# Kernel tuning notes

Hardware: AMD Instinct MI355X
Metric: run time of the kernel (lower is better)

## Reference

```python
import jax, jax.numpy as jnp
import numpy as np

# Dimensions derived from Mamba.__init__: d_model=512 -> joint_latent=32, mamb_latent=D=640
NL, D, DIN, DS, DTR, DC = 4, 640, 1280, 16, 40, 4  # n_layer, d_model, d_inner, d_state, dt_rank, d_conv
B, V = 64, 30  # batch, joint-sequence length (repeat_joint_num)


def _rms(x, w, eps=1e-5):
    return x * jax.lax.rsqrt(jnp.mean(x * x, axis=-1, keepdims=True) + eps) * w


def _mamba_block(x, in_w, conv_w, conv_b, xp_w, dt_w, dt_b, A_log, D_skip, out_w):
    # x: [B, V, D]
    u, res = jnp.split(jnp.einsum('bvd,ed->bve', x, in_w), 2, axis=-1)  # each [B,V,DIN]
    # causal depthwise conv1d over V
    xc = jnp.pad(u.transpose(0, 2, 1), ((0, 0), (0, 0), (DC - 1, 0)))  # [B,DIN,V+DC-1]
    xc = jax.lax.conv_general_dilated(xc, conv_w[:, None, :], (1,), 'VALID',
                                      feature_group_count=DIN,
                                      dimension_numbers=('NCH', 'OIH', 'NCH'))
    u = jax.nn.silu(xc.transpose(0, 2, 1) + conv_b)  # [B,V,DIN]
    # input-dependent SSM params
    dbl = jnp.einsum('bvd,ed->bve', u, xp_w)  # [B,V,DTR+2*DS]
    delta, Bm, Cm = jnp.split(dbl, [DTR, DTR + DS], axis=-1)
    delta = jax.nn.softplus(jnp.einsum('bvr,dr->bvd', delta, dt_w) + dt_b)  # [B,V,DIN]
    A = -jnp.exp(A_log)  # [DIN,DS]
    dA = jnp.exp(delta[..., None] * A)                              # [B,V,DIN,DS]
    dBu = delta[..., None] * Bm[:, :, None, :] * u[..., None]       # [B,V,DIN,DS]

    def step(h, t):
        dA_t, dBu_t, C_t = t
        h = dA_t * h + dBu_t                      # [B,DIN,DS]
        return h, jnp.einsum('bds,bs->bd', h, C_t)

    h0 = jnp.zeros((x.shape[0], DIN, DS), x.dtype)
    _, ys = jax.lax.scan(step, h0, (dA.transpose(1, 0, 2, 3),
                                    dBu.transpose(1, 0, 2, 3),
                                    Cm.transpose(1, 0, 2)))
    y = ys.transpose(1, 0, 2) + u * D_skip        # [B,V,DIN]
    return jnp.einsum('bvd,ed->bve', y * jax.nn.silu(res), out_w)


def setup_inputs() -> dict:
    key = jax.random.key(0)
    ks = jax.random.split(key, 10)
    s = 0.02
    return {
        'x': jax.random.normal(ks[0], (B, V, D), jnp.float32),
        'vs': jax.random.randint(ks[1], (B,), 0, V),
        'norm_w': jnp.ones((NL, D), jnp.float32),
        'in_proj_w': s * jax.random.normal(ks[2], (NL, 2 * DIN, D), jnp.float32),
        'conv_w': s * jax.random.normal(ks[3], (NL, DIN, DC), jnp.float32),
        'conv_b': jnp.zeros((NL, DIN), jnp.float32),
        'x_proj_w': s * jax.random.normal(ks[4], (NL, DTR + 2 * DS, DIN), jnp.float32),
        'dt_proj_w': s * jax.random.normal(ks[5], (NL, DIN, DTR), jnp.float32),
        'dt_proj_b': jnp.full((NL, DIN), -4.0, jnp.float32) + 0.1 * jax.random.normal(ks[6], (NL, DIN), jnp.float32),
        'A_log': jnp.tile(jnp.log(jnp.arange(1.0, DS + 1.0, dtype=jnp.float32)), (NL, DIN, 1)),
        'D_skip': jnp.ones((NL, DIN), jnp.float32),
        'out_proj_w': s * jax.random.normal(ks[7], (NL, D, DIN), jnp.float32),
        'norm_f_w': jnp.ones((D,), jnp.float32),
    }


def reference(x, vs, norm_w, in_proj_w, conv_w, conv_b, x_proj_w, dt_proj_w,
              dt_proj_b, A_log, D_skip, out_proj_w, norm_f_w):
    bidx = jnp.arange(x.shape[0])[:, None]
    # batch-wise circular permutation over V (circular_permute_v)
    fwd_idx = (jnp.arange(V)[None, :] + V - vs[:, None]) % V  # [B,V]
    h = x[bidx, fwd_idx]
    for i in range(NL):
        h = h + _mamba_block(_rms(h, norm_w[i]), in_proj_w[i], conv_w[i], conv_b[i],
                             x_proj_w[i], dt_proj_w[i], dt_proj_b[i], A_log[i],
                             D_skip[i], out_proj_w[i])
    h = _rms(h, norm_f_w)
    # reverse_circular_permute_v
    rev_idx = (jnp.arange(V)[None, :] + vs[:, None]) % V
    return h[bidx, rev_idx]
```

## Files before the change

kernel.cpp:

```cpp
#include <hip/hip_runtime.h>
#include <math.h>

#define NLAYER 4
#define DMODEL 640
#define DINNER 1280
#define DSTATE 16
#define DTRANK 40
#define DCONV  4
#define BATCH  64
#define SEQ    30
#define MTOK   (BATCH*SEQ)
#define NPROJ  (2*DINNER)
#define NDBL   (DTRANK+2*DSTATE)
#define NDBLP  80
#define KSEGS  8
#define KSEG   (DINNER/KSEGS)
#define DTKP   64

#define Q1 (NLAYER*NPROJ*DMODEL/4)
#define Q2 (NLAYER*DMODEL*DINNER/4)
#define Q3 (NLAYER*NDBLP*DINNER/4)
#define Q4 (NLAYER*DINNER*DTKP/4)
#define WCTOT (Q1+Q2+Q3+Q4)

typedef unsigned short u16;
typedef __bf16 bf16x8 __attribute__((ext_vector_type(8)));
typedef float  f32x4  __attribute__((ext_vector_type(4)));
typedef unsigned short u16x8 __attribute__((ext_vector_type(8)));

__device__ __forceinline__ float siluf(float x) {
    return x / (1.0f + __expf(-x));
}

__device__ __forceinline__ u16 f2bf(float f) {
    unsigned int u = __float_as_uint(f);
    u += 0x7fffu + ((u >> 16) & 1u);
    return (u16)(u >> 16);
}

__device__ __forceinline__ float bf2f(u16 b) {
    return __uint_as_float(((unsigned int)b) << 16);
}

__global__ void k_permute(const float* __restrict__ x, const int* __restrict__ vs,
                          float* __restrict__ h) {
    int idx = blockIdx.x * blockDim.x + threadIdx.x;
    if (idx >= MTOK * DMODEL) return;
    int d  = idx % DMODEL;
    int mv = idx / DMODEL;
    int v  = mv % SEQ;
    int b  = mv / SEQ;
    int src = (v + SEQ - vs[b]) % SEQ;
    h[idx] = x[(b * SEQ + src) * DMODEL + d];
}

__global__ __launch_bounds__(256)
void k_wconv(const float* __restrict__ in_w, const float* __restrict__ out_w,
             const float* __restrict__ xp_w, const float* __restrict__ dt_w,
             u16* __restrict__ wbi, u16* __restrict__ wbo,
             u16* __restrict__ wbx, u16* __restrict__ wdt) {
    int i = blockIdx.x * 256 + threadIdx.x;
    if (i < Q1) {
        int j = i * 4;
        float4 v = *(const float4*)(in_w + j);
        ushort4 o;
        o.x = f2bf(v.x); o.y = f2bf(v.y); o.z = f2bf(v.z); o.w = f2bf(v.w);
        *(ushort4*)(wbi + j) = o;
    } else if (i < Q1 + Q2) {
        int j = (i - Q1) * 4;
        float4 v = *(const float4*)(out_w + j);
        ushort4 o;
        o.x = f2bf(v.x); o.y = f2bf(v.y); o.z = f2bf(v.z); o.w = f2bf(v.w);
        *(ushort4*)(wbo + j) = o;
    } else if (i < Q1 + Q2 + Q3) {
        int j = (i - Q1 - Q2) * 4;
        int layer = j / (NDBLP * DINNER);
        int rem   = j % (NDBLP * DINNER);
        int r = rem / DINNER, c = rem % DINNER;
        ushort4 o = make_ushort4(0, 0, 0, 0);
        if (r < NDBL) {
            float4 v = *(const float4*)(xp_w + ((size_t)layer * NDBL + r) * DINNER + c);
            o.x = f2bf(v.x); o.y = f2bf(v.y); o.z = f2bf(v.z); o.w = f2bf(v.w);
        }
        *(ushort4*)(wbx + j) = o;
    } else {
        int j = (i - Q1 - Q2 - Q3) * 4;
        int ld = j / DTKP;
        int c  = j % DTKP;
        ushort4 o = make_ushort4(0, 0, 0, 0);
        if (c < DTRANK) {
            float4 v = *(const float4*)(dt_w + (size_t)ld * DTRANK + c);
            o.x = f2bf(v.x); o.y = f2bf(v.y); o.z = f2bf(v.z); o.w = f2bf(v.w);
        }
        *(ushort4*)(wdt + j) = o;
    }
}

__global__ __launch_bounds__(64)
void k_rmsnorm(const float* __restrict__ h, const float* __restrict__ w,
               u16* __restrict__ xn) {
    int m = blockIdx.x;
    int t = threadIdx.x;
    const float* row = h + (size_t)m * DMODEL;
    float2 vv[5];
    float ss = 0.f;
    #pragma unroll
    for (int i = 0; i < 5; ++i) {
        vv[i] = *(const float2*)(row + i * 128 + t * 2);
        ss += vv[i].x * vv[i].x + vv[i].y * vv[i].y;
    }
    #pragma unroll
    for (int o = 32; o > 0; o >>= 1) ss += __shfl_xor(ss, o, 64);
    float sc = rsqrtf(ss / DMODEL + 1e-5f);
    u16* outp = xn + (size_t)m * DMODEL;
    #pragma unroll
    for (int i = 0; i < 5; ++i) {
        int d = i * 128 + t * 2;
        float2 wv = *(const float2*)(w + d);
        ushort2 o;
        o.x = f2bf(vv[i].x * sc * wv.x);
        o.y = f2bf(vv[i].y * sc * wv.y);
        *(ushort2*)(outp + d) = o;
    }
}

__global__ __launch_bounds__(256)
void k_inproj(const u16* __restrict__ A, const u16* __restrict__ W,
              u16* __restrict__ Cb) {
    __shared__ u16 As[2][64 * 64];
    __shared__ u16 Bs[2][128 * 64];
    const int t = threadIdx.x;
    const int w = t >> 6, l = t & 63;
    const int lane15 = l & 15, quad = l >> 4;
    const int wm = w >> 1, wn = w & 1;
    const int m0 = blockIdx.y * 64, n0 = blockIdx.x * 128;

    f32x4 acc[2][4];
    #pragma unroll
    for (int i = 0; i < 2; ++i)
        #pragma unroll
        for (int j = 0; j < 4; ++j)
            acc[i][j] = (f32x4){0.f, 0.f, 0.f, 0.f};

    auto stage = [&](int buf, int k0) {
        #pragma unroll
        for (int q = 0; q < 2; ++q) {
            int c   = q * 256 + t;
            int row = c >> 3;
            int gch = ((c & 7) ^ (row & 7)) * 8;
            const u16* ga = A + (size_t)(m0 + row) * DMODEL + k0 + gch;
            __builtin_amdgcn_global_load_lds(
                (const __attribute__((address_space(1))) void*)ga,
                (__attribute__((address_space(3))) void*)&As[buf][c * 8], 16, 0, 0);
        }
        #pragma unroll
        for (int q = 0; q < 4; ++q) {
            int c   = q * 256 + t;
            int row = c >> 3;
            int gch = ((c & 7) ^ (row & 7)) * 8;
            const u16* gb = W + (size_t)(n0 + row) * DMODEL + k0 + gch;
            __builtin_amdgcn_global_load_lds(
                (const __attribute__((address_space(1))) void*)gb,
                (__attribute__((address_space(3))) void*)&Bs[buf][c * 8], 16, 0, 0);
        }
    };

    auto compute = [&](int buf) {
        #pragma unroll
        for (int ks = 0; ks < 2; ++ks) {
            bf16x8 af[2], bfr[4];
            #pragma unroll
            for (int i = 0; i < 2; ++i) {
                int row = wm * 32 + i * 16 + lane15;
                af[i] = *(const bf16x8*)&As[buf][row * 64 + (((ks * 4 + quad) ^ (row & 7)) * 8)];
            }
            #pragma unroll
            for (int j = 0; j < 4; ++j) {
                int row = wn * 64 + j * 16 + lane15;
                bfr[j] = *(const bf16x8*)&Bs[buf][row * 64 + (((ks * 4 + quad) ^ (row & 7)) * 8)];
            }
            #pragma unroll
            for (int i = 0; i < 2; ++i)
                #pragma unroll
                for (int j = 0; j < 4; ++j)
                    acc[i][j] = __builtin_amdgcn_mfma_f32_16x16x32_bf16(
                        af[i], bfr[j], acc[i][j], 0, 0, 0);
        }
    };

    const int NT = DMODEL / 64;
    stage(0, 0);
    __syncthreads();
    int cur = 0;
    for (int tt = 1; tt < NT; ++tt) {
        stage(cur ^ 1, tt * 64);
        compute(cur);
        __syncthreads();
        cur ^= 1;
    }
    compute(cur);

    #pragma unroll
    for (int i = 0; i < 2; ++i) {
        #pragma unroll
        for (int r = 0; r < 4; ++r) {
            int row = m0 + wm * 32 + i * 16 + quad * 4 + r;
            #pragma unroll
            for (int j = 0; j < 4; ++j) {
                int col = n0 + wn * 64 + j * 16 + lane15;
                Cb[(size_t)row * NPROJ + col] = f2bf(acc[i][j][r]);
            }
        }
    }
}

__global__ __launch_bounds__(128)
void k_outproj(const u16* __restrict__ A, const u16* __restrict__ W,
               const float* __restrict__ resid, float* __restrict__ C) {
    __shared__ u16 As[2][32 * 128];
    __shared__ u16 Bs[2][64 * 128];
    const int t = threadIdx.x;
    const int w = t >> 6, l = t & 63;
    const int lane15 = l & 15, quad = l >> 4;
    const int m0 = blockIdx.y * 32, n0 = blockIdx.x * 64;

    f32x4 acc[2][2];
    #pragma unroll
    for (int i = 0; i < 2; ++i)
        #pragma unroll
        for (int j = 0; j < 2; ++j)
            acc[i][j] = (f32x4){0.f, 0.f, 0.f, 0.f};

    auto stage = [&](int buf, int k0) {
        #pragma unroll
        for (int q = 0; q < 4; ++q) {
            int c   = q * 128 + t;
            int row = c >> 4;
            int gch = ((c & 15) ^ (row & 15)) * 8;
            const u16* ga = A + (size_t)(m0 + row) * DINNER + k0 + gch;
            __builtin_amdgcn_global_load_lds(
                (const __attribute__((address_space(1))) void*)ga,
                (__attribute__((address_space(3))) void*)&As[buf][c * 8], 16, 0, 0);
        }
        #pragma unroll
        for (int q = 0; q < 8; ++q) {
            int c   = q * 128 + t;
            int row = c >> 4;
            int gch = ((c & 15) ^ (row & 15)) * 8;
            const u16* gb = W + (size_t)(n0 + row) * DINNER + k0 + gch;
            __builtin_amdgcn_global_load_lds(
                (const __attribute__((address_space(1))) void*)gb,
                (__attribute__((address_space(3))) void*)&Bs[buf][c * 8], 16, 0, 0);
        }
    };

    auto compute = [&](int buf) {
        #pragma unroll
        for (int ks = 0; ks < 4; ++ks) {
            bf16x8 af[2], bfr[2];
            #pragma unroll
            for (int i = 0; i < 2; ++i) {
                int row = i * 16 + lane15;
                af[i] = *(const bf16x8*)&As[buf][row * 128 + (((ks * 4 + quad) ^ (row & 15)) * 8)];
            }
            #pragma unroll
            for (int j = 0; j < 2; ++j) {
                int row = w * 32 + j * 16 + lane15;
                bfr[j] = *(const bf16x8*)&Bs[buf][row * 128 + (((ks * 4 + quad) ^ (row & 15)) * 8)];
            }
            #pragma unroll
            for (int i = 0; i < 2; ++i)
                #pragma unroll
                for (int j = 0; j < 2; ++j)
                    acc[i][j] = __builtin_amdgcn_mfma_f32_16x16x32_bf16(
                        af[i], bfr[j], acc[i][j], 0, 0, 0);
        }
    };

    const int NT = DINNER / 128;
    stage(0, 0);
    __syncthreads();
    int cur = 0;
    for (int tt = 1; tt < NT; ++tt) {
        stage(cur ^ 1, tt * 128);
        compute(cur);
        __syncthreads();
        cur ^= 1;
    }
    compute(cur);

    #pragma unroll
    for (int i = 0; i < 2; ++i) {
        #pragma unroll
        for (int r = 0; r < 4; ++r) {
            int row = m0 + i * 16 + quad * 4 + r;
            #pragma unroll
            for (int j = 0; j < 2; ++j) {
                int col = n0 + w * 32 + j * 16 + lane15;
                size_t idx = (size_t)row * DMODEL + col;
                C[idx] = acc[i][j][r] + resid[idx];
            }
        }
    }
}

__global__ __launch_bounds__(256)
void k_conv(const u16* __restrict__ urb, const float* __restrict__ cw,
            const float* __restrict__ cb, u16* __restrict__ ubf) {
    int idx = blockIdx.x * 256 + threadIdx.x;
    int c = idx % DINNER;
    int b = idx / DINNER;
    const u16* up = urb + (size_t)(b * SEQ) * NPROJ + c;
    float xv[SEQ];
    #pragma unroll
    for (int v = 0; v < SEQ; ++v) xv[v] = bf2f(up[(size_t)v * NPROJ]);
    float w0 = cw[c * 4 + 0], w1 = cw[c * 4 + 1];
    float w2 = cw[c * 4 + 2], w3 = cw[c * 4 + 3];
    float bias = cb[c];
    u16* op = ubf + (size_t)(b * SEQ) * DINNER + c;
    float x0 = 0.f, x1 = 0.f, x2 = 0.f;
    #pragma unroll
    for (int v = 0; v < SEQ; ++v) {
        float x3 = xv[v];
        float o = bias + w0 * x0 + w1 * x1 + w2 * x2 + w3 * x3;
        op[(size_t)v * DINNER] = f2bf(siluf(o));
        x0 = x1; x1 = x2; x2 = x3;
    }
}

__global__ __launch_bounds__(256)
void k_xproj(const u16* __restrict__ ubf, const u16* __restrict__ wbx,
             float* __restrict__ dblp) {
    __shared__ u16 As[64 * KSEG];
    __shared__ u16 Bs[NDBLP * KSEG];
    const int t = threadIdx.x;
    const int w = t >> 6, l = t & 63;
    const int lane15 = l & 15, quad = l >> 4;
    const int seg = blockIdx.x;
    const int m0 = blockIdx.y * 64;
    const int kb = seg * KSEG;

    #pragma unroll
    for (int q = 0; q < 5; ++q) {
        int c   = q * 256 + t;
        int row = c / 20, ch = c - row * 20;
        const u16* ga = ubf + (size_t)(m0 + row) * DINNER + kb + ch * 8;
        __builtin_amdgcn_global_load_lds(
            (const __attribute__((address_space(1))) void*)ga,
            (__attribute__((address_space(3))) void*)&As[c * 8], 16, 0, 0);
    }
    #pragma unroll
    for (int q = 0; q < 6; ++q) {
        int c   = q * 256 + t;
        int row = c / 20, ch = c - row * 20;
        const u16* gb = wbx + (size_t)row * DINNER + kb + ch * 8;
        __builtin_amdgcn_global_load_lds(
            (const __attribute__((address_space(1))) void*)gb,
            (__attribute__((address_space(3))) void*)&Bs[c * 8], 16, 0, 0);
    }
    if (t < 64) {
        int c   = 1536 + t;
        int row = c / 20, ch = c - row * 20;
        const u16* gb = wbx + (size_t)row * DINNER + kb + ch * 8;
        __builtin_amdgcn_global_load_lds(
            (const __attribute__((address_space(1))) void*)gb,
            (__attribute__((address_space(3))) void*)&Bs[c * 8], 16, 0, 0);
    }
    __syncthreads();

    f32x4 acc[5];
    #pragma unroll
    for (int j = 0; j < 5; ++j) acc[j] = (f32x4){0.f, 0.f, 0.f, 0.f};

    #pragma unroll
    for (int k0 = 0; k0 < KSEG; k0 += 32) {
        bf16x8 af = *(const bf16x8*)&As[(w * 16 + lane15) * KSEG + k0 + quad * 8];
        #pragma unroll
        for (int j = 0; j < 5; ++j) {
            bf16x8 bfrag = *(const bf16x8*)&Bs[(j * 16 + lane15) * KSEG + k0 + quad * 8];
            acc[j] = __builtin_amdgcn_mfma_f32_16x16x32_bf16(af, bfrag, acc[j], 0, 0, 0);
        }
    }

    float* outp = dblp + (size_t)seg * MTOK * NDBLP;
    #pragma unroll
    for (int r = 0; r < 4; ++r) {
        int row = m0 + w * 16 + quad * 4 + r;
        #pragma unroll
        for (int j = 0; j < 5; ++j) {
            int col = j * 16 + lane15;
            outp[(size_t)row * NDBLP + col] = acc[j][r];
        }
    }
}

__global__ __launch_bounds__(256)
void k_dtgemm(const float* __restrict__ dblp, const u16* __restrict__ dtwb,
              const float* __restrict__ dtb, u16* __restrict__ delta) {
    __shared__ u16 As[2][64 * 32];
    __shared__ u16 Bs[2][64 * 32];
    const int t = threadIdx.x;
    const int w = t >> 6, l = t & 63;
    const int lane15 = l & 15, quad = l >> 4;
    const int wm = w >> 1, wn = w & 1;
    const int m0 = blockIdx.y * 64, n0 = blockIdx.x * 64;
    const int row = t >> 2, koff = (t & 3) * 8;
    const int m = m0 + row;

    #pragma unroll
    for (int kt = 0; kt < 2; ++kt) {
        int c = t;
        const u16* gb = dtwb + (size_t)(n0 + (c >> 2)) * DTKP + kt * 32 + (c & 3) * 8;
        __builtin_amdgcn_global_load_lds(
            (const __attribute__((address_space(1))) void*)gb,
            (__attribute__((address_space(3))) void*)&Bs[kt][c * 8], 16, 0, 0);
    }

    float sums[2][8];
    #pragma unroll
    for (int kt = 0; kt < 2; ++kt)
        #pragma unroll
        for (int e = 0; e < 8; ++e) sums[kt][e] = 0.f;
    #pragma unroll
    for (int kt = 0; kt < 2; ++kt) {
        #pragma unroll
        for (int q = 0; q < 2; ++q) {
            int col = kt * 32 + koff + q * 4;
            if (col < DTRANK) {
                #pragma unroll
                for (int sg = 0; sg < KSEGS; ++sg) {
                    float4 p = *(const float4*)&dblp[(size_t)sg * MTOK * NDBLP
                                                     + (size_t)m * NDBLP + col];
                    sums[kt][q * 4 + 0] += p.x; sums[kt][q * 4 + 1] += p.y;
                    sums[kt][q * 4 + 2] += p.z; sums[kt][q * 4 + 3] += p.w;
                }
            }
        }
    }
    #pragma unroll
    for (int kt = 0; kt < 2; ++kt) {
        u16x8 av;
        #pragma unroll
        for (int e = 0; e < 8; ++e) av[e] = f2bf(sums[kt][e]);
        *(u16x8*)&As[kt][row * 32 + koff] = av;
    }
    __syncthreads();

    f32x4 acc[2][2];
    #pragma unroll
    for (int i = 0; i < 2; ++i)
        #pragma unroll
        for (int j = 0; j < 2; ++j)
            acc[i][j] = (f32x4){0.f, 0.f, 0.f, 0.f};

    #pragma unroll
    for (int kt = 0; kt < 2; ++kt) {
        bf16x8 af[2], bfrag[2];
        #pragma unroll
        for (int i = 0; i < 2; ++i)
            af[i] = *(const bf16x8*)&As[kt][(wm * 32 + i * 16 + lane15) * 32 + quad * 8];
        #pragma unroll
        for (int j = 0; j < 2; ++j)
            bfrag[j] = *(const bf16x8*)&Bs[kt][(wn * 32 + j * 16 + lane15) * 32 + quad * 8];
        #pragma unroll
        for (int i = 0; i < 2; ++i)
            #pragma unroll
            for (int j = 0; j < 2; ++j)
                acc[i][j] = __builtin_amdgcn_mfma_f32_16x16x32_bf16(
                    af[i], bfrag[j], acc[i][j], 0, 0, 0);
    }

    #pragma unroll
    for (int i = 0; i < 2; ++i) {
        #pragma unroll
        for (int r = 0; r < 4; ++r) {
            int orow = m0 + wm * 32 + i * 16 + quad * 4 + r;
            #pragma unroll
            for (int j = 0; j < 2; ++j) {
                int col = n0 + wn * 32 + j * 16 + lane15;
                float vv = acc[i][j][r] + dtb[col];
                vv = (vv > 20.f) ? vv : log1pf(__expf(vv));
                delta[(size_t)orow * DINNER + col] = f2bf(vv);
            }
        }
    }
}

__global__ __launch_bounds__(256)
void k_scan(const u16* __restrict__ ubf, const u16* __restrict__ urb,
            const float* __restrict__ dblp, const u16* __restrict__ delta,
            const float* __restrict__ A_log, const float* __restrict__ Dsk,
            u16* __restrict__ y) {
    __shared__ float BC[SEQ][2 * DSTATE];
    const int b  = blockIdx.x / (DINNER / 128);
    const int dc = blockIdx.x % (DINNER / 128);
    const int dloc = threadIdx.x >> 1;
    const int half = threadIdx.x & 1;
    const int d  = dc * 128 + dloc;

    for (int t = threadIdx.x; t < SEQ * 2 * DSTATE; t += 256) {
        int v = t >> 5, s = t & 31;
        float acc = 0.f;
        #pragma unroll
        for (int sg = 0; sg < KSEGS; ++sg)
            acc += dblp[(size_t)sg * MTOK * NDBLP + (size_t)(b * SEQ + v) * NDBLP + DTRANK + s];
        BC[v][s] = acc;
    }
    __syncthreads();

    float dl[SEQ], uu[SEQ], rr[SEQ];
    #pragma unroll
    for (int v = 0; v < SEQ; ++v)
        dl[v] = bf2f(delta[(size_t)(b * SEQ + v) * DINNER + d]);
    #pragma unroll
    for (int v = 0; v < SEQ; ++v)
        uu[v] = bf2f(ubf[(size_t)(b * SEQ + v) * DINNER + d]);
    #pragma unroll
    for (int v = 0; v < SEQ; ++v)
        rr[v] = bf2f(urb[(size_t)(b * SEQ + v) * NPROJ + DINNER + d]);

    float Ar[8];
    #pragma unroll
    for (int s = 0; s < 8; ++s)
        Ar[s] = -__expf(A_log[(size_t)d * DSTATE + half * 8 + s]);
    float dsk = Dsk[d];
    float st8[8];
    #pragma unroll
    for (int s = 0; s < 8; ++s) st8[s] = 0.f;

    u16* yp = y + (size_t)(b * SEQ) * DINNER + d;

    #pragma unroll
    for (int v = 0; v < SEQ; ++v) {
        float dlt = dl[v];
        float du  = dlt * uu[v];
        float ya = 0.f, yb = 0.f;
        #pragma unroll
        for (int s = 0; s < 8; s += 4) {
            float dA0 = __expf(dlt * Ar[s + 0]);
            float dA1 = __expf(dlt * Ar[s + 1]);
            float dA2 = __expf(dlt * Ar[s + 2]);
            float dA3 = __expf(dlt * Ar[s + 3]);
            st8[s + 0] = dA0 * st8[s + 0] + du * BC[v][half * 8 + s + 0];
            st8[s + 1] = dA1 * st8[s + 1] + du * BC[v][half * 8 + s + 1];
            st8[s + 2] = dA2 * st8[s + 2] + du * BC[v][half * 8 + s + 2];
            st8[s + 3] = dA3 * st8[s + 3] + du * BC[v][half * 8 + s + 3];
            ya += st8[s + 0] * BC[v][DSTATE + half * 8 + s + 0];
            yb += st8[s + 1] * BC[v][DSTATE + half * 8 + s + 1];
            ya += st8[s + 2] * BC[v][DSTATE + half * 8 + s + 2];
            yb += st8[s + 3] * BC[v][DSTATE + half * 8 + s + 3];
        }
        float yh = ya + yb;
        yh += __shfl_xor(yh, 1, 64);
        if (half == 0)
            yp[(size_t)v * DINNER] = f2bf((yh + uu[v] * dsk) * siluf(rr[v]));
    }
}

__global__ __launch_bounds__(64)
void k_final(const float* __restrict__ h, const int* __restrict__ vs,
             const float* __restrict__ w, float* __restrict__ out) {
    int mv = blockIdx.x;
    int v = mv % SEQ, b = mv / SEQ;
    int src = (v + vs[b]) % SEQ;
    const float* row = h + (size_t)(b * SEQ + src) * DMODEL;
    int t = threadIdx.x;
    float ss = 0.f;
    for (int d = t; d < DMODEL; d += 64) { float x = row[d]; ss += x * x; }
    #pragma unroll
    for (int o = 32; o > 0; o >>= 1) ss += __shfl_xor(ss, o, 64);
    float sc = rsqrtf(ss / DMODEL + 1e-5f);
    float* op = out + (size_t)mv * DMODEL;
    for (int d = t; d < DMODEL; d += 64) op[d] = row[d] * sc * w[d];
}

extern "C" void kernel_launch(void* const* d_in, const int* in_sizes, int n_in,
                              void* d_out, int out_size, void* d_ws, size_t ws_size,
                              hipStream_t stream) {
    const float* x      = (const float*)d_in[0];
    const int*   vs     = (const int*)d_in[1];
    const float* norm_w = (const float*)d_in[2];
    const float* in_w   = (const float*)d_in[3];
    const float* conv_w = (const float*)d_in[4];
    const float* conv_b = (const float*)d_in[5];
    const float* xp_w   = (const float*)d_in[6];
    const float* dt_w   = (const float*)d_in[7];
    const float* dt_b   = (const float*)d_in[8];
    const float* A_log  = (const float*)d_in[9];
    const float* Dsk    = (const float*)d_in[10];
    const float* out_w  = (const float*)d_in[11];
    const float* nfw    = (const float*)d_in[12];
    float* out = (float*)d_out;

    char* p = (char*)d_ws;
    float* h      = (float*)p; p += (size_t)MTOK * DMODEL * 4;
    u16*   xn     = (u16*)p;   p += (size_t)MTOK * DMODEL * 2;
    u16*   urb    = (u16*)p;   p += (size_t)MTOK * NPROJ * 2;
    u16*   ubf    = (u16*)p;   p += (size_t)MTOK * DINNER * 2;
    float* dblp   = (float*)p; p += (size_t)KSEGS * MTOK * NDBLP * 4;
    u16*   deltab = (u16*)p;   p += (size_t)MTOK * DINNER * 2;
    u16*   y      = (u16*)p;   p += (size_t)MTOK * DINNER * 2;
    u16*   wbi4   = (u16*)p;   p += (size_t)NLAYER * NPROJ * DMODEL * 2;
    u16*   wbo4   = (u16*)p;   p += (size_t)NLAYER * DMODEL * DINNER * 2;
    u16*   wbx4   = (u16*)p;   p += (size_t)NLAYER * NDBLP * DINNER * 2;
    u16*   wdt4   = (u16*)p;   p += (size_t)NLAYER * DINNER * DTKP * 2;

    k_wconv<<<WCTOT / 256, 256, 0, stream>>>(
        in_w, out_w, xp_w, dt_w, wbi4, wbo4, wbx4, wdt4);

    k_permute<<<(MTOK * DMODEL + 255) / 256, 256, 0, stream>>>(x, vs, h);

    for (int l = 0; l < NLAYER; ++l) {
        k_rmsnorm<<<MTOK, 64, 0, stream>>>(h, norm_w + (size_t)l * DMODEL, xn);

        k_inproj<<<dim3(NPROJ / 128, MTOK / 64), 256, 0, stream>>>(
            xn, wbi4 + (size_t)l * NPROJ * DMODEL, urb);

        k_conv<<<BATCH * DINNER / 256, 256, 0, stream>>>(
            urb, conv_w + (size_t)l * DINNER * DCONV, conv_b + (size_t)l * DINNER, ubf);

        k_xproj<<<dim3(KSEGS, MTOK / 64), 256, 0, stream>>>(
            ubf, wbx4 + (size_t)l * NDBLP * DINNER, dblp);

        k_dtgemm<<<dim3(DINNER / 64, MTOK / 64), 256, 0, stream>>>(
            dblp, wdt4 + (size_t)l * DINNER * DTKP,
            dt_b + (size_t)l * DINNER, deltab);

        k_scan<<<BATCH * (DINNER / 128), 256, 0, stream>>>(
            ubf, urb, dblp, deltab,
            A_log + (size_t)l * DINNER * DSTATE, Dsk + (size_t)l * DINNER, y);

        k_outproj<<<dim3(DMODEL / 64, MTOK / 32), 128, 0, stream>>>(
            y, wbo4 + (size_t)l * DMODEL * DINNER, h, h);
    }

    k_final<<<MTOK, 64, 0, stream>>>(h, vs, nfw, out);
}
```

Before: 441.4 us.

## Fuse dt-projection GEMM with selective scan into one kernel

Merges the dt_proj GEMM (with softplus) and the selective-scan kernel into a single kernel, so each block computes delta for 60 tokens (two batches) by 64 channels and keeps it in shared memory. The scan then reads delta, u and the gate res from LDS instead of global memory, and the bf16 delta buffer is removed. This saves one launch plus the write and re-read of delta. In exchange each block uses more LDS, the GEMM runs on 60 valid rows padded to 64 (clamped row index), and the grid shape changes.

```diff
diff --git a/kernel.cpp b/kernel.cpp
--- a/kernel.cpp
+++ b/kernel.cpp
@@ -395,17 +395,25 @@
 }
 
 __global__ __launch_bounds__(256)
-void k_dtgemm(const float* __restrict__ dblp, const u16* __restrict__ dtwb,
-              const float* __restrict__ dtb, u16* __restrict__ delta) {
+void k_dtscan(const float* __restrict__ dblp, const u16* __restrict__ dtwb,
+              const float* __restrict__ dtb,
+              const u16* __restrict__ ubf, const u16* __restrict__ urb,
+              const float* __restrict__ A_log, const float* __restrict__ Dsk,
+              u16* __restrict__ y) {
     __shared__ u16 As[2][64 * 32];
     __shared__ u16 Bs[2][64 * 32];
+    __shared__ u16 ldelta[64][64];
+    __shared__ float BC2[2][SEQ][32];
+    __shared__ u16 UU[60 * 64];
+    __shared__ u16 RR[60 * 64];
     const int t = threadIdx.x;
     const int w = t >> 6, l = t & 63;
     const int lane15 = l & 15, quad = l >> 4;
     const int wm = w >> 1, wn = w & 1;
-    const int m0 = blockIdx.y * 64, n0 = blockIdx.x * 64;
+    const int n0 = blockIdx.x * 64;
+    const int m0 = blockIdx.y * 60;
     const int row = t >> 2, koff = (t & 3) * 8;
-    const int m = m0 + row;
+    const int mm = min(m0 + row, MTOK - 1);
 
     #pragma unroll
     for (int kt = 0; kt < 2; ++kt) {
@@ -415,6 +423,28 @@
             (const __attribute__((address_space(1))) void*)gb,
             (__attribute__((address_space(3))) void*)&Bs[kt][c * 8], 16, 0, 0);
     }
+    for (int o = t; o < 480; o += 256) {
+        int rr_ = o >> 3, ch = o & 7;
+        const u16* g1 = ubf + (size_t)(m0 + rr_) * DINNER + n0 + ch * 8;
+        __builtin_amdgcn_global_load_lds(
+            (const __attribute__((address_space(1))) void*)g1,
+            (__attribute__((address_space(3))) void*)&UU[o * 8], 16, 0, 0);
+        const u16* g2 = urb + (size_t)(m0 + rr_) * NPROJ + DINNER + n0 + ch * 8;
+        __builtin_amdgcn_global_load_lds(
+            (const __attribute__((address_space(1))) void*)g2,
+            (__attribute__((address_space(3))) void*)&RR[o * 8], 16, 0, 0);
+    }
+    for (int s0 = t; s0 < 2 * SEQ * 32; s0 += 256) {
+        int lb  = s0 / (SEQ * 32);
+        int rem = s0 - lb * SEQ * 32;
+        int v = rem >> 5, st = rem & 31;
+        int token = m0 + lb * SEQ + v;
+        float a = 0.f;
+        #pragma unroll
+        for (int sg = 0; sg < KSEGS; ++sg)
+            a += dblp[(size_t)sg * MTOK * NDBLP + (size_t)token * NDBLP + DTRANK + st];
+        BC2[lb][v][st] = a;
+    }
 
     float sums[2][8];
     #pragma unroll
@@ -430,7 +460,7 @@
                 #pragma unroll
                 for (int sg = 0; sg < KSEGS; ++sg) {
                     float4 p = *(const float4*)&dblp[(size_t)sg * MTOK * NDBLP
-                                                     + (size_t)m * NDBLP + col];
+                                                     + (size_t)mm * NDBLP + col];
                     sums[kt][q * 4 + 0] += p.x; sums[kt][q * 4 + 1] += p.y;
                     sums[kt][q * 4 + 2] += p.z; sums[kt][q * 4 + 3] += p.w;
                 }
@@ -474,50 +504,23 @@
     for (int i = 0; i < 2; ++i) {
         #pragma unroll
         for (int r = 0; r < 4; ++r) {
-            int orow = m0 + wm * 32 + i * 16 + quad * 4 + r;
+            int orow = wm * 32 + i * 16 + quad * 4 + r;
             #pragma unroll
             for (int j = 0; j < 2; ++j) {
-                int col = n0 + wn * 32 + j * 16 + lane15;
-                float vv = acc[i][j][r] + dtb[col];
+                int col = wn * 32 + j * 16 + lane15;
+                float vv = acc[i][j][r] + dtb[n0 + col];
                 vv = (vv > 20.f) ? vv : log1pf(__expf(vv));
-                delta[(size_t)orow * DINNER + col] = f2bf(vv);
-            }
-        }
-    }
-}
-
-__global__ __launch_bounds__(256)
-void k_scan(const u16* __restrict__ ubf, const u16* __restrict__ urb,
-            const float* __restrict__ dblp, const u16* __restrict__ delta,
-            const float* __restrict__ A_log, const float* __restrict__ Dsk,
-            u16* __restrict__ y) {
-    __shared__ float BC[SEQ][2 * DSTATE];
-    const int b  = blockIdx.x / (DINNER / 128);
-    const int dc = blockIdx.x % (DINNER / 128);
-    const int dloc = threadIdx.x >> 1;
-    const int half = threadIdx.x & 1;
-    const int d  = dc * 128 + dloc;
-
-    for (int t = threadIdx.x; t < SEQ * 2 * DSTATE; t += 256) {
-        int v = t >> 5, s = t & 31;
-        float acc = 0.f;
-        #pragma unroll
-        for (int sg = 0; sg < KSEGS; ++sg)
-            acc += dblp[(size_t)sg * MTOK * NDBLP + (size_t)(b * SEQ + v) * NDBLP + DTRANK + s];
-        BC[v][s] = acc;
+                ldelta[orow][col] = f2bf(vv);
+            }
+        }
     }
     __syncthreads();
 
-    float dl[SEQ], uu[SEQ], rr[SEQ];
-    #pragma unroll
-    for (int v = 0; v < SEQ; ++v)
-        dl[v] = bf2f(delta[(size_t)(b * SEQ + v) * DINNER + d]);
-    #pragma unroll
-    for (int v = 0; v < SEQ; ++v)
-        uu[v] = bf2f(ubf[(size_t)(b * SEQ + v) * DINNER + d]);
-    #pragma unroll
-    for (int v = 0; v < SEQ; ++v)
-        rr[v] = bf2f(urb[(size_t)(b * SEQ + v) * NPROJ + DINNER + d]);
+    const int lb   = t >> 7;
+    const int dloc = (t >> 1) & 63;
+    const int half = t & 1;
+    const int d    = n0 + dloc;
+    const int b    = m0 / SEQ + lb;
 
     float Ar[8];
     #pragma unroll
@@ -532,8 +535,9 @@
 
     #pragma unroll
     for (int v = 0; v < SEQ; ++v) {
-        float dlt = dl[v];
-        float du  = dlt * uu[v];
+        float dlt = bf2f(ldelta[lb * SEQ + v][dloc]);
+        float u   = bf2f(UU[(lb * SEQ + v) * 64 + dloc]);
+        float du  = dlt * u;
         float ya = 0.f, yb = 0.f;
         #pragma unroll
         for (int s = 0; s < 8; s += 4) {
@@ -541,19 +545,21 @@
             float dA1 = __expf(dlt * Ar[s + 1]);
             float dA2 = __expf(dlt * Ar[s + 2]);
             float dA3 = __expf(dlt * Ar[s + 3]);
-            st8[s + 0] = dA0 * st8[s + 0] + du * BC[v][half * 8 + s + 0];
-            st8[s + 1] = dA1 * st8[s + 1] + du * BC[v][half * 8 + s + 1];
-            st8[s + 2] = dA2 * st8[s + 2] + du * BC[v][half * 8 + s + 2];
-            st8[s + 3] = dA3 * st8[s + 3] + du * BC[v][half * 8 + s + 3];
-            ya += st8[s + 0] * BC[v][DSTATE + half * 8 + s + 0];
-            yb += st8[s + 1] * BC[v][DSTATE + half * 8 + s + 1];
-            ya += st8[s + 2] * BC[v][DSTATE + half * 8 + s + 2];
-            yb += st8[s + 3] * BC[v][DSTATE + half * 8 + s + 3];
+            st8[s + 0] = dA0 * st8[s + 0] + du * BC2[lb][v][half * 8 + s + 0];
+            st8[s + 1] = dA1 * st8[s + 1] + du * BC2[lb][v][half * 8 + s + 1];
+            st8[s + 2] = dA2 * st8[s + 2] + du * BC2[lb][v][half * 8 + s + 2];
+            st8[s + 3] = dA3 * st8[s + 3] + du * BC2[lb][v][half * 8 + s + 3];
+            ya += st8[s + 0] * BC2[lb][v][DSTATE + half * 8 + s + 0];
+            yb += st8[s + 1] * BC2[lb][v][DSTATE + half * 8 + s + 1];
+            ya += st8[s + 2] * BC2[lb][v][DSTATE + half * 8 + s + 2];
+            yb += st8[s + 3] * BC2[lb][v][DSTATE + half * 8 + s + 3];
         }
         float yh = ya + yb;
         yh += __shfl_xor(yh, 1, 64);
-        if (half == 0)
-            yp[(size_t)v * DINNER] = f2bf((yh + uu[v] * dsk) * siluf(rr[v]));
+        if (half == 0) {
+            float r = bf2f(RR[(lb * SEQ + v) * 64 + dloc]);
+            yp[(size_t)v * DINNER] = f2bf((yh + u * dsk) * siluf(r));
+        }
     }
 }
 
@@ -598,7 +604,6 @@
     u16*   urb    = (u16*)p;   p += (size_t)MTOK * NPROJ * 2;
     u16*   ubf    = (u16*)p;   p += (size_t)MTOK * DINNER * 2;
     float* dblp   = (float*)p; p += (size_t)KSEGS * MTOK * NDBLP * 4;
-    u16*   deltab = (u16*)p;   p += (size_t)MTOK * DINNER * 2;
     u16*   y      = (u16*)p;   p += (size_t)MTOK * DINNER * 2;
     u16*   wbi4   = (u16*)p;   p += (size_t)NLAYER * NPROJ * DMODEL * 2;
     u16*   wbo4   = (u16*)p;   p += (size_t)NLAYER * DMODEL * DINNER * 2;
@@ -622,13 +627,9 @@
         k_xproj<<<dim3(KSEGS, MTOK / 64), 256, 0, stream>>>(
             ubf, wbx4 + (size_t)l * NDBLP * DINNER, dblp);
 
-        k_dtgemm<<<dim3(DINNER / 64, MTOK / 64), 256, 0, stream>>>(
-            dblp, wdt4 + (size_t)l * DINNER * DTKP,
-            dt_b + (size_t)l * DINNER, deltab);
-
-        k_scan<<<BATCH * (DINNER / 128), 256, 0, stream>>>(
-            ubf, urb, dblp, deltab,
-            A_log + (size_t)l * DINNER * DSTATE, Dsk + (size_t)l * DINNER, y);
+        k_dtscan<<<dim3(DINNER / 64, MTOK / 60), 256, 0, stream>>>(
+            dblp, wdt4 + (size_t)l * DINNER * DTKP, dt_b + (size_t)l * DINNER,
+            ubf, urb, A_log + (size_t)l * DINNER * DSTATE, Dsk + (size_t)l * DINNER, y);
 
         k_outproj<<<dim3(DMODEL / 64, MTOK / 32), 128, 0, stream>>>(
             y, wbo4 + (size_t)l * DMODEL * DINNER, h, h);
```

Result: no change. 435.1 us (-1.4%).
